# Performance work log

Hardware: AMD Instinct MI355X
Metric: run time of the kernel (lower is better)

The kernel has to match this reference:

```python
import jax, jax.numpy as jnp
from jax import lax
import numpy as np

EPS = 1e-5


def setup_inputs() -> dict:
    key = jax.random.key(0)
    ks = jax.random.split(key, 12)
    S, N, C, V = 512, 64, 512, 10
    sc = 1.0 / np.sqrt(C)
    inp = {
        "memory": jax.random.normal(ks[0], (S, N, C), jnp.float32),
        "W_act": jax.random.normal(ks[1], (C, 2), jnp.float32) * sc,
        "b_act": jnp.zeros((2,), jnp.float32),
        "W_ih": jax.random.normal(ks[2], (4 * C, C), jnp.float32) * sc,
        "W_hh": jax.random.normal(ks[3], (4 * C, C), jnp.float32) * sc,
        "b_ih": jnp.zeros((4 * C,), jnp.float32),
        "b_hh": jnp.zeros((4 * C,), jnp.float32),
        "ln_gamma": jnp.ones((C,), jnp.float32),
        "ln_beta": jnp.zeros((C,), jnp.float32),
        "W_dec": jax.random.normal(ks[4], (C, V), jnp.float32) * sc,
        "b_dec": jnp.zeros((V,), jnp.float32),
        "qsize": 256,
    }
    return inp


def reference(memory, W_act, b_act, W_ih, W_hh, b_ih, b_hh,
              ln_gamma, ln_beta, W_dec, b_dec, qsize):
    S, N, C = memory.shape
    # action probabilities (training path: plain softmax), [S, N, 2]
    actions = jax.nn.softmax(memory @ W_act + b_act, axis=-1)

    # posvec linear recurrence: p_{i+1} = p_i * a0_i + roll(p_i, 1) * a1_i
    p0 = jnp.zeros((qsize, N), memory.dtype).at[0].set(1.0)

    def pos_step(p, a):  # a: [N, 2]
        p_next = p * a[:, 0] + jnp.roll(p, 1, axis=0) * a[:, 1]
        return p_next, p  # emit posvec BEFORE update (used at step i)

    _, posvecs = lax.scan(pos_step, p0, actions)  # [S, qsize, N]

    # queue = sum_i outer(posvec_i, memory_i) * a1_i  -> [qsize, N, C]
    queue = jnp.einsum('sqn,snc,sn->qnc', posvecs, memory, actions[..., 1])

    # single-layer LSTM over the queue dimension (PyTorch gate order i,f,g,o)
    h0 = jnp.zeros((N, C), memory.dtype)

    def lstm_step(carry, x):  # x: [N, C]
        h, c = carry
        gates = x @ W_ih.T + h @ W_hh.T + b_ih + b_hh  # [N, 4C]
        i, f, g, o = jnp.split(gates, 4, axis=-1)
        c = jax.nn.sigmoid(f) * c + jax.nn.sigmoid(i) * jnp.tanh(g)
        h = jax.nn.sigmoid(o) * jnp.tanh(c)
        return (h, c), h

    _, hs = lax.scan(lstm_step, (h0, h0), queue)  # [qsize, N, C]

    # dropout is identity in eval / reference mode
    mu = jnp.mean(hs, axis=-1, keepdims=True)
    var = jnp.mean(jnp.square(hs - mu), axis=-1, keepdims=True)
    normed = (hs - mu) * lax.rsqrt(var + EPS) * ln_gamma + ln_beta

    return normed @ W_dec + b_dec  # [qsize, N, V]
```

## Files before the change

### kernel.cpp

```cpp
#include <hip/hip_runtime.h>
#include <hip/hip_bf16.h>

typedef __bf16 bf16;
typedef __bf16 bf16x8 __attribute__((ext_vector_type(8)));
typedef float f32x4 __attribute__((ext_vector_type(4)));
typedef float f32x16 __attribute__((ext_vector_type(16)));

#define S_ 512
#define N_ 64
#define C_ 512
#define V_ 10
#define Q_ 256

#define OFF_A0   ((size_t)0)
#define OFF_A1   (OFF_A0 + (size_t)S_ * N_ * 4)
#define OFF_PW   (OFF_A1 + (size_t)S_ * N_ * 4)
#define OFF_QU   (OFF_PW + (size_t)N_ * Q_ * S_ * 2)
#define OFF_H    (OFF_QU + (size_t)Q_ * N_ * C_ * 2)
#define OFF_HS   (OFF_H + (size_t)2 * N_ * C_ * 2)
#define OFF_BAR  (OFF_HS + (size_t)Q_ * N_ * C_ * 2)

__device__ __forceinline__ float sigf(float x) { return 1.f / (1.f + __expf(-x)); }
__device__ __forceinline__ float tanhf_(float x) { return 1.f - 2.f / (__expf(2.f * x) + 1.f); }

__global__ __launch_bounds__(256) void k_actions(const float* __restrict__ mem,
    const float* __restrict__ Wact, const float* __restrict__ bact,
    float* __restrict__ A0, float* __restrict__ A1) {
  const int wid = threadIdx.x >> 6, lane = threadIdx.x & 63;
  const int row = blockIdx.x * 4 + wid;
  const int s = row >> 6, n = row & 63;
  const float* mrow = mem + (size_t)row * C_ + lane * 8;
  const float* wrow = Wact + (size_t)lane * 16;
  float4 m0 = *(const float4*)(mrow);
  float4 m1 = *(const float4*)(mrow + 4);
  float d0 = 0.f, d1 = 0.f;
  float mv[8] = {m0.x, m0.y, m0.z, m0.w, m1.x, m1.y, m1.z, m1.w};
#pragma unroll
  for (int j = 0; j < 8; ++j) {
    d0 += mv[j] * wrow[j * 2 + 0];
    d1 += mv[j] * wrow[j * 2 + 1];
  }
#pragma unroll
  for (int m = 32; m >= 1; m >>= 1) {
    d0 += __shfl_xor(d0, m);
    d1 += __shfl_xor(d1, m);
  }
  if (lane == 0) {
    float l0 = d0 + bact[0], l1 = d1 + bact[1];
    float mx = fmaxf(l0, l1);
    float e0 = __expf(l0 - mx), e1 = __expf(l1 - mx);
    float inv = 1.f / (e0 + e1);
    A0[(size_t)n * S_ + s] = e0 * inv;
    A1[(size_t)n * S_ + s] = e1 * inv;
  }
}

__global__ __launch_bounds__(256) void k_posvec(const float* __restrict__ A0,
    const float* __restrict__ A1, bf16* __restrict__ Pw) {
  __shared__ float a0s[S_], a1s[S_];
  __shared__ float pbuf[2][Q_];
  const int n = blockIdx.x, t = threadIdx.x;
  a0s[t] = A0[(size_t)n * S_ + t];
  a0s[t + 256] = A0[(size_t)n * S_ + t + 256];
  a1s[t] = A1[(size_t)n * S_ + t];
  a1s[t + 256] = A1[(size_t)n * S_ + t + 256];
  float p = (t == 0) ? 1.f : 0.f;
  __syncthreads();
  for (int s8 = 0; s8 < S_; s8 += 8) {
    float emit[8];
#pragma unroll
    for (int jj = 0; jj < 8; ++jj) {
      const int s = s8 + jj;
      pbuf[jj & 1][t] = p;
      __syncthreads();
      float pm1 = pbuf[jj & 1][(t + Q_ - 1) & (Q_ - 1)];
      float a0 = a0s[s], a1 = a1s[s];
      emit[jj] = p * a1;
      p = fmaf(pm1, a1, p * a0);
    }
    bf16x8 v;
#pragma unroll
    for (int jj = 0; jj < 8; ++jj) v[jj] = (bf16)emit[jj];
    *(bf16x8*)(Pw + ((size_t)n * Q_ + t) * S_ + s8) = v;
  }
}

__global__ __launch_bounds__(256) void k_queue(const bf16* __restrict__ Pw,
    const float* __restrict__ mem, bf16* __restrict__ qout) {
  __shared__ bf16 bt[64 * 32];
  const int bid = blockIdx.x;
  const int n = bid >> 5, qt = (bid >> 3) & 3, ct = bid & 7;
  const int q0 = qt * 64, c0 = ct * 64;
  const int t = threadIdx.x, wid = t >> 6, lane = t & 63;
  const int lrow = lane & 15, lkb = lane >> 4;
  f32x4 acc[4] = {};
  const bf16* arow = Pw + ((size_t)n * Q_ + q0 + wid * 16 + lrow) * S_ + lkb * 8;
  const int sl = t >> 3, cb = (t & 7) * 8;
  const float* msrc = mem + ((size_t)sl * N_ + n) * C_ + c0 + cb;
  for (int kb = 0; kb < 16; ++kb) {
    float4 f0 = *(const float4*)(msrc + (size_t)kb * 32 * N_ * C_);
    float4 f1 = *(const float4*)(msrc + (size_t)kb * 32 * N_ * C_ + 4);
    __syncthreads();
    float fv[8] = {f0.x, f0.y, f0.z, f0.w, f1.x, f1.y, f1.z, f1.w};
#pragma unroll
    for (int jw = 0; jw < 8; ++jw) {
      const int row = cb + jw;
      bt[row * 32 + ((((sl >> 3) ^ (row & 3)) << 3) | (sl & 7))] = (bf16)fv[jw];
    }
    __syncthreads();
    bf16x8 a = *(const bf16x8*)(arow + kb * 32);
#pragma unroll
    for (int cs = 0; cs < 4; ++cs) {
      const int row = cs * 16 + lrow;
      bf16x8 b = *(const bf16x8*)(&bt[row * 32 + ((lkb ^ (row & 3)) << 3)]);
      acc[cs] = __builtin_amdgcn_mfma_f32_16x16x32_bf16(a, b, acc[cs], 0, 0, 0);
    }
  }
#pragma unroll
  for (int cs = 0; cs < 4; ++cs) {
#pragma unroll
    for (int r = 0; r < 4; ++r) {
      const int q = q0 + wid * 16 + (lane >> 4) * 4 + r;
      const int c = c0 + cs * 16 + lrow;
      qout[((size_t)q * N_ + n) * C_ + c] = (bf16)acc[cs][r];
    }
  }
}

__global__ __launch_bounds__(256, 1) void k_lstm(
    const bf16* __restrict__ queue, const float* __restrict__ Wih,
    const float* __restrict__ Whh, const float* __restrict__ bih,
    const float* __restrict__ bhh, bf16* __restrict__ H,
    bf16* __restrict__ hs, int* __restrict__ ctrl) {
  const int bid = blockIdx.x, t = threadIdx.x;

  if (bid >= 64) {
    float x0 = 1.f + t, x1 = 2.f + t, x2 = 3.f + t, x3 = 4.f + t;
    for (int outer = 0; outer < 10000; ++outer) {
      int d;
      asm volatile("global_load_dword %0, %1, off sc0 sc1" : "=v"(d) : "v"(ctrl));
#pragma unroll
      for (int i = 0; i < 500; ++i) {
        x0 = fmaf(x0, 0.9999999f, 1e-7f);
        x1 = fmaf(x1, 0.9999998f, 2e-7f);
        x2 = fmaf(x2, 1.0000001f, 3e-7f);
        x3 = fmaf(x3, 1.0000002f, 4e-7f);
      }
      asm volatile("s_waitcnt vmcnt(0)" ::: "memory");
      if (d) break;
    }
    asm volatile("" :: "v"(x0), "v"(x1), "v"(x2), "v"(x3));
    return;
  }

  __shared__ float gx[2][2][32][33];
  __shared__ float gh[2][32][33];
  __shared__ float bias[32];
  __shared__ int ldsCnt[Q_];
  __shared__ int ldsCnt0;
  int* flags = ctrl + 64;
  const int w = bid;
  const int wid = t >> 6, lane = t & 63;
  const int mat = wid >> 1;
  const int blk = wid & 1;

  const int col = lane & 31;
  const int kg = (lane >> 5) * 8;
  const int wr = (col & 3) * 512 + w * 8 + (col >> 2);
  const float* Wsrc = (mat ? Whh : Wih) + (size_t)wr * C_ + kg;
  bf16x8 bw[32];
#pragma unroll
  for (int kb = 0; kb < 32; ++kb) {
    float4 wa = *(const float4*)(Wsrc + kb * 16);
    float4 wb = *(const float4*)(Wsrc + kb * 16 + 4);
    bf16x8 v;
    v[0] = (bf16)wa.x; v[1] = (bf16)wa.y; v[2] = (bf16)wa.z; v[3] = (bf16)wa.w;
    v[4] = (bf16)wb.x; v[5] = (bf16)wb.y; v[6] = (bf16)wb.z; v[7] = (bf16)wb.w;
    bw[kb] = v;
  }
  if (t < 32) {
    const int rr = (t & 3) * 512 + w * 8 + (t >> 2);
    bias[t] = bih[rr] + bhh[rr];
  }
  ldsCnt[t] = 0;
  if (t == 0) ldsCnt0 = 0;
  __syncthreads();

  const int en = t >> 2, ep = t & 3;
  {
    unsigned* Hp = (unsigned*)H + ((size_t)0 * N_ + en) * (C_ / 2) + w * 4 + ep;
    unsigned z = 0;
    asm volatile("global_store_dword %0, %1, off sc0 sc1" :: "v"(Hp), "v"(z) : "memory");
    asm volatile("s_waitcnt vmcnt(0)" ::: "memory");
    if (lane == 0) {
      if (atomicAdd(&ldsCnt0, 1) == 3) {
        int one = 1;
        int* fp = flags + w;
        asm volatile("global_store_dword %0, %1, off sc0 sc1" :: "v"(fp), "v"(one) : "memory");
      }
    }
  }

  float cs0 = 0.f, cs1 = 0.f;
  const int eb = en >> 5, er = en & 31, j0 = ep * 8;

  bf16x8 xf[32];
  if (mat == 0) {
    const bf16* xb = queue + ((size_t)0 * N_ + blk * 32 + (lane & 31)) * C_ + kg;
#pragma unroll
    for (int kb = 0; kb < 32; ++kb) xf[kb] = *(const bf16x8*)(xb + kb * 16);
    {
      f32x16 acc[4] = {};
#pragma unroll
      for (int kb = 0; kb < 32; ++kb)
        acc[kb & 3] = __builtin_amdgcn_mfma_f32_32x32x16_bf16(xf[kb], bw[kb], acc[kb & 3], 0, 0, 0);
      f32x16 asum = (acc[0] + acc[1]) + (acc[2] + acc[3]);
#pragma unroll
      for (int rg = 0; rg < 16; ++rg) {
        const int rl = (rg & 3) + 8 * (rg >> 2) + 4 * (lane >> 5);
        gx[0][blk][rl][col] = asum[rg];
      }
    }
    const bf16* xb1 = queue + ((size_t)1 * N_ + blk * 32 + (lane & 31)) * C_ + kg;
#pragma unroll
    for (int kb = 0; kb < 32; ++kb) xf[kb] = *(const bf16x8*)(xb1 + kb * 16);
  }

  for (int step = 0; step < Q_; ++step) {
    const int p = step & 1;
    const int cur = p, nxt = p ^ 1;
    if (mat == 1) {
      {
        int v;
        int* fa = flags + lane;
        do {
          asm volatile("global_load_dword %0, %1, off sc0 sc1" : "=v"(v) : "v"(fa));
          asm volatile("s_waitcnt vmcnt(0)" ::: "memory");
        } while (!__all(v >= step + 1));
      }
      __builtin_amdgcn_sched_barrier(0);
      const bf16* hb = H + ((size_t)cur * N_ + blk * 32 + (lane & 31)) * C_ + kg;
      bf16x8 hf[32];
#pragma unroll
      for (int kb = 0; kb < 32; ++kb)
        asm volatile("global_load_dwordx4 %0, %1, off offset:%2 sc0 sc1"
                     : "=v"(hf[kb]) : "v"(hb), "i"(kb * 32));
      f32x16 acc[4] = {};
      asm volatile("s_waitcnt vmcnt(24)" ::: "memory");
      __builtin_amdgcn_sched_barrier(0);
#pragma unroll
      for (int kb = 0; kb < 8; ++kb)
        acc[kb & 3] = __builtin_amdgcn_mfma_f32_32x32x16_bf16(hf[kb], bw[kb], acc[kb & 3], 0, 0, 0);
      asm volatile("s_waitcnt vmcnt(16)" ::: "memory");
      __builtin_amdgcn_sched_barrier(0);
#pragma unroll
      for (int kb = 8; kb < 16; ++kb)
        acc[kb & 3] = __builtin_amdgcn_mfma_f32_32x32x16_bf16(hf[kb], bw[kb], acc[kb & 3], 0, 0, 0);
      asm volatile("s_waitcnt vmcnt(8)" ::: "memory");
      __builtin_amdgcn_sched_barrier(0);
#pragma unroll
      for (int kb = 16; kb < 24; ++kb)
        acc[kb & 3] = __builtin_amdgcn_mfma_f32_32x32x16_bf16(hf[kb], bw[kb], acc[kb & 3], 0, 0, 0);
      asm volatile("s_waitcnt vmcnt(0)" ::: "memory");
      __builtin_amdgcn_sched_barrier(0);
#pragma unroll
      for (int kb = 24; kb < 32; ++kb)
        acc[kb & 3] = __builtin_amdgcn_mfma_f32_32x32x16_bf16(hf[kb], bw[kb], acc[kb & 3], 0, 0, 0);
      f32x16 asum = (acc[0] + acc[1]) + (acc[2] + acc[3]);
#pragma unroll
      for (int rg = 0; rg < 16; ++rg) {
        const int rl = (rg & 3) + 8 * (rg >> 2) + 4 * (lane >> 5);
        gh[blk][rl][col] = asum[rg];
      }
    } else if (step + 1 < Q_) {
      f32x16 acc[4] = {};
#pragma unroll
      for (int kb = 0; kb < 32; ++kb)
        acc[kb & 3] = __builtin_amdgcn_mfma_f32_32x32x16_bf16(xf[kb], bw[kb], acc[kb & 3], 0, 0, 0);
      f32x16 asum = (acc[0] + acc[1]) + (acc[2] + acc[3]);
#pragma unroll
      for (int rg = 0; rg < 16; ++rg) {
        const int rl = (rg & 3) + 8 * (rg >> 2) + 4 * (lane >> 5);
        gx[p ^ 1][blk][rl][col] = asum[rg];
      }
    }
    __syncthreads();

    {
      float g0 = gx[p][eb][er][j0 + 0] + gh[eb][er][j0 + 0] + bias[j0 + 0];
      float g1 = gx[p][eb][er][j0 + 1] + gh[eb][er][j0 + 1] + bias[j0 + 1];
      float g2 = gx[p][eb][er][j0 + 2] + gh[eb][er][j0 + 2] + bias[j0 + 2];
      float g3 = gx[p][eb][er][j0 + 3] + gh[eb][er][j0 + 3] + bias[j0 + 3];
      cs0 = sigf(g1) * cs0 + sigf(g0) * tanhf_(g2);
      float h0v = sigf(g3) * tanhf_(cs0);
      float g4 = gx[p][eb][er][j0 + 4] + gh[eb][er][j0 + 4] + bias[j0 + 4];
      float g5 = gx[p][eb][er][j0 + 5] + gh[eb][er][j0 + 5] + bias[j0 + 5];
      float g6 = gx[p][eb][er][j0 + 6] + gh[eb][er][j0 + 6] + bias[j0 + 6];
      float g7 = gx[p][eb][er][j0 + 7] + gh[eb][er][j0 + 7] + bias[j0 + 7];
      cs1 = sigf(g5) * cs1 + sigf(g4) * tanhf_(g6);
      float h1v = sigf(g7) * tanhf_(cs1);
      unsigned lo = __builtin_bit_cast(unsigned short, (bf16)h0v);
      unsigned hi = __builtin_bit_cast(unsigned short, (bf16)h1v);
      unsigned hp = (hi << 16) | lo;
      unsigned* Hp = (unsigned*)H + ((size_t)nxt * N_ + en) * (C_ / 2) + w * 4 + ep;
      asm volatile("global_store_dword %0, %1, off sc0 sc1" :: "v"(Hp), "v"(hp) : "memory");
      *((unsigned*)hs + ((size_t)step * N_ + en) * (C_ / 2) + w * 4 + ep) = hp;
    }
    asm volatile("s_waitcnt vmcnt(1)" ::: "memory");
    if (step + 1 < Q_) {
      if (lane == 0) {
        if (atomicAdd(&ldsCnt[step], 1) == 3) {
          int fv = step + 2;
          int* fp = flags + w;
          asm volatile("global_store_dword %0, %1, off sc0 sc1" :: "v"(fp), "v"(fv) : "memory");
        }
      }
      if (mat == 0 && step + 2 < Q_) {
        const bf16* xb = queue + ((size_t)(step + 2) * N_ + blk * 32 + (lane & 31)) * C_ + kg;
#pragma unroll
        for (int kb = 0; kb < 32; ++kb) xf[kb] = *(const bf16x8*)(xb + kb * 16);
      }
    }
    __syncthreads();
  }

  if (t == 0 && bid == 0) {
    int one = 1;
    asm volatile("global_store_dword %0, %1, off sc0 sc1" :: "v"(ctrl), "v"(one) : "memory");
  }
}

__global__ __launch_bounds__(256) void k_lndec(const bf16* __restrict__ hs,
    const float* __restrict__ gamma, const float* __restrict__ beta,
    const float* __restrict__ Wdec, const float* __restrict__ bdec,
    float* __restrict__ out) {
  const int wid = threadIdx.x >> 6, lane = threadIdx.x & 63;
  const int row = blockIdx.x * 4 + wid;
  const bf16* hrow = hs + (size_t)row * C_ + lane * 8;
  bf16x8 hv = *(const bf16x8*)hrow;
  float h[8];
  float sm = 0.f, sq = 0.f;
#pragma unroll
  for (int j = 0; j < 8; ++j) {
    h[j] = (float)hv[j];
    sm += h[j];
    sq += h[j] * h[j];
  }
#pragma unroll
  for (int m = 32; m >= 1; m >>= 1) {
    sm += __shfl_xor(sm, m);
    sq += __shfl_xor(sq, m);
  }
  const float mu = sm * (1.f / C_);
  const float var = sq * (1.f / C_) - mu * mu;
  const float rs = 1.f / sqrtf(var + 1e-5f);
  float o[V_] = {};
#pragma unroll
  for (int j = 0; j < 8; ++j) {
    const int cj = lane * 8 + j;
    const float nv = (h[j] - mu) * rs * gamma[cj] + beta[cj];
    const float* wr = Wdec + (size_t)cj * V_;
#pragma unroll
    for (int v = 0; v < V_; ++v) o[v] += nv * wr[v];
  }
#pragma unroll
  for (int v = 0; v < V_; ++v) {
#pragma unroll
    for (int m = 32; m >= 1; m >>= 1) o[v] += __shfl_xor(o[v], m);
  }
  if (lane == 0) {
#pragma unroll
    for (int v = 0; v < V_; ++v) out[(size_t)row * V_ + v] = o[v] + bdec[v];
  }
}

extern "C" void kernel_launch(void* const* d_in, const int* in_sizes, int n_in,
                              void* d_out, int out_size, void* d_ws, size_t ws_size,
                              hipStream_t stream) {
  (void)in_sizes; (void)n_in; (void)out_size; (void)ws_size;
  const float* mem  = (const float*)d_in[0];
  const float* Wact = (const float*)d_in[1];
  const float* bact = (const float*)d_in[2];
  const float* Wih  = (const float*)d_in[3];
  const float* Whh  = (const float*)d_in[4];
  const float* bih  = (const float*)d_in[5];
  const float* bhh  = (const float*)d_in[6];
  const float* gam  = (const float*)d_in[7];
  const float* bet  = (const float*)d_in[8];
  const float* Wdec = (const float*)d_in[9];
  const float* bdec = (const float*)d_in[10];
  float* out = (float*)d_out;

  char* ws = (char*)d_ws;
  float* A0 = (float*)(ws + OFF_A0);
  float* A1 = (float*)(ws + OFF_A1);
  bf16* Pw  = (bf16*)(ws + OFF_PW);
  bf16* qu  = (bf16*)(ws + OFF_QU);
  bf16* H   = (bf16*)(ws + OFF_H);
  bf16* hs  = (bf16*)(ws + OFF_HS);
  int* ctrl = (int*)(ws + OFF_BAR);

  hipMemsetAsync(ctrl, 0, 4096, stream);
  k_actions<<<(S_ * N_) / 4, 256, 0, stream>>>(mem, Wact, bact, A0, A1);
  k_posvec<<<N_, 256, 0, stream>>>(A0, A1, Pw);
  k_queue<<<N_ * 32, 256, 0, stream>>>(Pw, mem, qu);
  k_lstm<<<256, 256, 0, stream>>>(qu, Wih, Whh, bih, bhh, H, hs, ctrl);
  k_lndec<<<(Q_ * N_) / 4, 256, 0, stream>>>(hs, gam, bet, Wdec, bdec, out);
}
```

Baseline: 1.675 ms.

## Replace LSTM step flags with step-tagged hidden-state words and chunked validation

The hidden state is now stored as 32-bit words, each carrying a bf16 value in the low half and the step number in the high half. Consumer warps load it in double-buffered chunks and re-issue a chunk until every tag matches, instead of waiting on a per-step flag and then fetching the data. This removes one global round trip per recurrence step; the remaining per-block progress counter is only a coarse hint, and its spin loop is now bounded. The 192 busy-spinning filler blocks are removed and the grid shrinks to 64 blocks, which may change clock behaviour. The trade-off is doubled hidden-state traffic and fewer MFMA accumulator chains.

```diff
diff --git a/kernel.cpp b/kernel.cpp
--- a/kernel.cpp
+++ b/kernel.cpp
@@ -16,9 +16,9 @@
 #define OFF_A1   (OFF_A0 + (size_t)S_ * N_ * 4)
 #define OFF_PW   (OFF_A1 + (size_t)S_ * N_ * 4)
 #define OFF_QU   (OFF_PW + (size_t)N_ * Q_ * S_ * 2)
-#define OFF_H    (OFF_QU + (size_t)Q_ * N_ * C_ * 2)
-#define OFF_HS   (OFF_H + (size_t)2 * N_ * C_ * 2)
-#define OFF_BAR  (OFF_HS + (size_t)Q_ * N_ * C_ * 2)
+#define OFF_HP   (OFF_QU + (size_t)Q_ * N_ * C_ * 2)
+#define OFF_HS   (OFF_HP + (size_t)2 * N_ * C_ * 4)
+#define OFF_CTRL (OFF_HS + (size_t)Q_ * N_ * C_ * 2)
 
 __device__ __forceinline__ float sigf(float x) { return 1.f / (1.f + __expf(-x)); }
 __device__ __forceinline__ float tanhf_(float x) { return 1.f - 2.f / (__expf(2.f * x) + 1.f); }
@@ -127,39 +127,68 @@
   }
 }
 
+
+#define ISSUE_CHUNK(BUF, C8)                                                    \
+  {                                                                             \
+    _Pragma("unroll") for (int i_ = 0; i_ < 8; ++i_)                            \
+        asm volatile("global_load_dwordx4 %0, %1, off offset:%2 sc0 sc1"        \
+                     : "=v"(BUF[i_])                                            \
+                     : "v"(hb), "i"(((C8) * 4 + (i_ >> 1)) * 64 + (i_ & 1) * 16)); \
+  }
+
+#define CHECK_CHUNK(BUF, OKV)                                                   \
+  {                                                                             \
+    unsigned a_ = 0;                                                            \
+    _Pragma("unroll") for (int i_ = 0; i_ < 8; ++i_) {                          \
+      a_ |= (BUF[i_].x ^ want); a_ |= (BUF[i_].y ^ want);                       \
+      a_ |= (BUF[i_].z ^ want); a_ |= (BUF[i_].w ^ want);                       \
+    }                                                                           \
+    OKV = (a_ < 0x10000u);                                                      \
+  }
+
+#define CONSUME_CHUNK(BUF, C8)                                                  \
+  {                                                                             \
+    _Pragma("unroll") for (int k_ = 0; k_ < 4; ++k_) {                          \
+      union { unsigned u[4]; bf16x8 v; } cv_;                                   \
+      cv_.u[0] = (BUF[k_ * 2].y << 16) | (BUF[k_ * 2].x & 0xffffu);             \
+      cv_.u[1] = (BUF[k_ * 2].w << 16) | (BUF[k_ * 2].z & 0xffffu);             \
+      cv_.u[2] = (BUF[k_ * 2 + 1].y << 16) | (BUF[k_ * 2 + 1].x & 0xffffu);     \
+      cv_.u[3] = (BUF[k_ * 2 + 1].w << 16) | (BUF[k_ * 2 + 1].z & 0xffffu);     \
+      const int kb_ = (C8) * 4 + k_;                                            \
+      acc[kb_ & 1] = __builtin_amdgcn_mfma_f32_32x32x16_bf16(cv_.v, bw[kb_],    \
+                                                             acc[kb_ & 1], 0, 0, 0); \
+    }                                                                           \
+  }
+
+#define CHUNK_STEP(C8, X, Y)                                                    \
+  {                                                                             \
+    if ((C8) < 7) {                                                             \
+      ISSUE_CHUNK(Y, (C8) + 1);                                                 \
+      asm volatile("s_waitcnt vmcnt(8)" ::: "memory");                          \
+    } else {                                                                    \
+      asm volatile("s_waitcnt vmcnt(0)" ::: "memory");                          \
+    }                                                                           \
+    __builtin_amdgcn_sched_barrier(0);                                          \
+    int ok_;                                                                    \
+    CHECK_CHUNK(X, ok_);                                                        \
+    while (!__all(ok_)) {                                                       \
+      ISSUE_CHUNK(X, C8);                                                       \
+      asm volatile("s_waitcnt vmcnt(0)" ::: "memory");                          \
+      __builtin_amdgcn_sched_barrier(0);                                        \
+      CHECK_CHUNK(X, ok_);                                                      \
+    }                                                                           \
+    CONSUME_CHUNK(X, C8)                                                        \
+  }
+
 __global__ __launch_bounds__(256, 1) void k_lstm(
     const bf16* __restrict__ queue, const float* __restrict__ Wih,
     const float* __restrict__ Whh, const float* __restrict__ bih,
-    const float* __restrict__ bhh, bf16* __restrict__ H,
-    bf16* __restrict__ hs, int* __restrict__ ctrl) {
-  const int bid = blockIdx.x, t = threadIdx.x;
-
-  if (bid >= 64) {
-    float x0 = 1.f + t, x1 = 2.f + t, x2 = 3.f + t, x3 = 4.f + t;
-    for (int outer = 0; outer < 10000; ++outer) {
-      int d;
-      asm volatile("global_load_dword %0, %1, off sc0 sc1" : "=v"(d) : "v"(ctrl));
-#pragma unroll
-      for (int i = 0; i < 500; ++i) {
-        x0 = fmaf(x0, 0.9999999f, 1e-7f);
-        x1 = fmaf(x1, 0.9999998f, 2e-7f);
-        x2 = fmaf(x2, 1.0000001f, 3e-7f);
-        x3 = fmaf(x3, 1.0000002f, 4e-7f);
-      }
-      asm volatile("s_waitcnt vmcnt(0)" ::: "memory");
-      if (d) break;
-    }
-    asm volatile("" :: "v"(x0), "v"(x1), "v"(x2), "v"(x3));
-    return;
-  }
-
+    const float* __restrict__ bhh, unsigned* __restrict__ Hp,
+    bf16* __restrict__ hs, int* __restrict__ summ) {
   __shared__ float gx[2][2][32][33];
   __shared__ float gh[2][32][33];
   __shared__ float bias[32];
-  __shared__ int ldsCnt[Q_];
-  __shared__ int ldsCnt0;
-  int* flags = ctrl + 64;
-  const int w = bid;
+  const int w = blockIdx.x, t = threadIdx.x;
   const int wid = t >> 6, lane = t & 63;
   const int mat = wid >> 1;
   const int blk = wid & 1;
@@ -182,23 +211,16 @@
     const int rr = (t & 3) * 512 + w * 8 + (t >> 2);
     bias[t] = bih[rr] + bhh[rr];
   }
-  ldsCnt[t] = 0;
-  if (t == 0) ldsCnt0 = 0;
-  __syncthreads();
 
   const int en = t >> 2, ep = t & 3;
   {
-    unsigned* Hp = (unsigned*)H + ((size_t)0 * N_ + en) * (C_ / 2) + w * 4 + ep;
-    unsigned z = 0;
-    asm volatile("global_store_dword %0, %1, off sc0 sc1" :: "v"(Hp), "v"(z) : "memory");
+    uint2 z0; z0.x = 0u; z0.y = 0u;
+    uint2 z1; z1.x = 0xFFFF0000u; z1.y = 0xFFFF0000u;
+    unsigned* p0 = Hp + ((size_t)0 * N_ + en) * C_ + w * 8 + ep * 2;
+    unsigned* p1 = Hp + ((size_t)1 * N_ + en) * C_ + w * 8 + ep * 2;
+    asm volatile("global_store_dwordx2 %0, %1, off sc0 sc1" :: "v"(p0), "v"(z0) : "memory");
+    asm volatile("global_store_dwordx2 %0, %1, off sc0 sc1" :: "v"(p1), "v"(z1) : "memory");
     asm volatile("s_waitcnt vmcnt(0)" ::: "memory");
-    if (lane == 0) {
-      if (atomicAdd(&ldsCnt0, 1) == 3) {
-        int one = 1;
-        int* fp = flags + w;
-        asm volatile("global_store_dword %0, %1, off sc0 sc1" :: "v"(fp), "v"(one) : "memory");
-      }
-    }
   }
 
   float cs0 = 0.f, cs1 = 0.f;
@@ -210,11 +232,11 @@
 #pragma unroll
     for (int kb = 0; kb < 32; ++kb) xf[kb] = *(const bf16x8*)(xb + kb * 16);
     {
-      f32x16 acc[4] = {};
+      f32x16 acc[2] = {};
 #pragma unroll
       for (int kb = 0; kb < 32; ++kb)
-        acc[kb & 3] = __builtin_amdgcn_mfma_f32_32x32x16_bf16(xf[kb], bw[kb], acc[kb & 3], 0, 0, 0);
-      f32x16 asum = (acc[0] + acc[1]) + (acc[2] + acc[3]);
+        acc[kb & 1] = __builtin_amdgcn_mfma_f32_32x32x16_bf16(xf[kb], bw[kb], acc[kb & 1], 0, 0, 0);
+      f32x16 asum = acc[0] + acc[1];
 #pragma unroll
       for (int rg = 0; rg < 16; ++rg) {
         const int rl = (rg & 3) + 8 * (rg >> 2) + 4 * (lane >> 5);
@@ -231,53 +253,39 @@
     const int cur = p, nxt = p ^ 1;
     if (mat == 1) {
       {
-        int v;
-        int* fa = flags + lane;
+        int v, it = 0;
+        const int* fa = summ + lane;
         do {
           asm volatile("global_load_dword %0, %1, off sc0 sc1" : "=v"(v) : "v"(fa));
           asm volatile("s_waitcnt vmcnt(0)" ::: "memory");
-        } while (!__all(v >= step + 1));
+        } while (__any(v < step) && ++it < 16384);
       }
       __builtin_amdgcn_sched_barrier(0);
-      const bf16* hb = H + ((size_t)cur * N_ + blk * 32 + (lane & 31)) * C_ + kg;
-      bf16x8 hf[32];
-#pragma unroll
-      for (int kb = 0; kb < 32; ++kb)
-        asm volatile("global_load_dwordx4 %0, %1, off offset:%2 sc0 sc1"
-                     : "=v"(hf[kb]) : "v"(hb), "i"(kb * 32));
-      f32x16 acc[4] = {};
-      asm volatile("s_waitcnt vmcnt(24)" ::: "memory");
-      __builtin_amdgcn_sched_barrier(0);
-#pragma unroll
-      for (int kb = 0; kb < 8; ++kb)
-        acc[kb & 3] = __builtin_amdgcn_mfma_f32_32x32x16_bf16(hf[kb], bw[kb], acc[kb & 3], 0, 0, 0);
-      asm volatile("s_waitcnt vmcnt(16)" ::: "memory");
-      __builtin_amdgcn_sched_barrier(0);
-#pragma unroll
-      for (int kb = 8; kb < 16; ++kb)
-        acc[kb & 3] = __builtin_amdgcn_mfma_f32_32x32x16_bf16(hf[kb], bw[kb], acc[kb & 3], 0, 0, 0);
-      asm volatile("s_waitcnt vmcnt(8)" ::: "memory");
-      __builtin_amdgcn_sched_barrier(0);
-#pragma unroll
-      for (int kb = 16; kb < 24; ++kb)
-        acc[kb & 3] = __builtin_amdgcn_mfma_f32_32x32x16_bf16(hf[kb], bw[kb], acc[kb & 3], 0, 0, 0);
-      asm volatile("s_waitcnt vmcnt(0)" ::: "memory");
-      __builtin_amdgcn_sched_barrier(0);
-#pragma unroll
-      for (int kb = 24; kb < 32; ++kb)
-        acc[kb & 3] = __builtin_amdgcn_mfma_f32_32x32x16_bf16(hf[kb], bw[kb], acc[kb & 3], 0, 0, 0);
-      f32x16 asum = (acc[0] + acc[1]) + (acc[2] + acc[3]);
+      const unsigned want = (unsigned)step << 16;
+      unsigned* hb = Hp + ((size_t)cur * N_ + blk * 32 + (lane & 31)) * C_ + kg;
+      f32x16 acc[2] = {};
+      uint4 ba[8], bb[8];
+      ISSUE_CHUNK(ba, 0);
+      CHUNK_STEP(0, ba, bb);
+      CHUNK_STEP(1, bb, ba);
+      CHUNK_STEP(2, ba, bb);
+      CHUNK_STEP(3, bb, ba);
+      CHUNK_STEP(4, ba, bb);
+      CHUNK_STEP(5, bb, ba);
+      CHUNK_STEP(6, ba, bb);
+      CHUNK_STEP(7, bb, ba);
+      f32x16 asum = acc[0] + acc[1];
 #pragma unroll
       for (int rg = 0; rg < 16; ++rg) {
         const int rl = (rg & 3) + 8 * (rg >> 2) + 4 * (lane >> 5);
         gh[blk][rl][col] = asum[rg];
       }
     } else if (step + 1 < Q_) {
-      f32x16 acc[4] = {};
+      f32x16 acc[2] = {};
 #pragma unroll
       for (int kb = 0; kb < 32; ++kb)
-        acc[kb & 3] = __builtin_amdgcn_mfma_f32_32x32x16_bf16(xf[kb], bw[kb], acc[kb & 3], 0, 0, 0);
-      f32x16 asum = (acc[0] + acc[1]) + (acc[2] + acc[3]);
+        acc[kb & 1] = __builtin_amdgcn_mfma_f32_32x32x16_bf16(xf[kb], bw[kb], acc[kb & 1], 0, 0, 0);
+      f32x16 asum = acc[0] + acc[1];
 #pragma unroll
       for (int rg = 0; rg < 16; ++rg) {
         const int rl = (rg & 3) + 8 * (rg >> 2) + 4 * (lane >> 5);
@@ -299,34 +307,24 @@
       float g7 = gx[p][eb][er][j0 + 7] + gh[eb][er][j0 + 7] + bias[j0 + 7];
       cs1 = sigf(g5) * cs1 + sigf(g4) * tanhf_(g6);
       float h1v = sigf(g7) * tanhf_(cs1);
-      unsigned lo = __builtin_bit_cast(unsigned short, (bf16)h0v);
-      unsigned hi = __builtin_bit_cast(unsigned short, (bf16)h1v);
-      unsigned hp = (hi << 16) | lo;
-      unsigned* Hp = (unsigned*)H + ((size_t)nxt * N_ + en) * (C_ / 2) + w * 4 + ep;
-      asm volatile("global_store_dword %0, %1, off sc0 sc1" :: "v"(Hp), "v"(hp) : "memory");
-      *((unsigned*)hs + ((size_t)step * N_ + en) * (C_ / 2) + w * 4 + ep) = hp;
-    }
-    asm volatile("s_waitcnt vmcnt(1)" ::: "memory");
-    if (step + 1 < Q_) {
-      if (lane == 0) {
-        if (atomicAdd(&ldsCnt[step], 1) == 3) {
-          int fv = step + 2;
-          int* fp = flags + w;
-          asm volatile("global_store_dword %0, %1, off sc0 sc1" :: "v"(fp), "v"(fv) : "memory");
-        }
-      }
-      if (mat == 0 && step + 2 < Q_) {
-        const bf16* xb = queue + ((size_t)(step + 2) * N_ + blk * 32 + (lane & 31)) * C_ + kg;
-#pragma unroll
-        for (int kb = 0; kb < 32; ++kb) xf[kb] = *(const bf16x8*)(xb + kb * 16);
-      }
+      unsigned lo = (unsigned)__builtin_bit_cast(unsigned short, (bf16)h0v);
+      unsigned hi = (unsigned)__builtin_bit_cast(unsigned short, (bf16)h1v);
+      const unsigned tagv = (unsigned)(step + 1) << 16;
+      uint2 pr; pr.x = tagv | lo; pr.y = tagv | hi;
+      unsigned* Hq = Hp + ((size_t)nxt * N_ + en) * C_ + w * 8 + ep * 2;
+      asm volatile("global_store_dwordx2 %0, %1, off sc0 sc1" :: "v"(Hq), "v"(pr) : "memory");
+      *((unsigned*)hs + ((size_t)step * N_ + en) * (C_ / 2) + w * 4 + ep) = (hi << 16) | lo;
+    }
+    if (mat == 0 && step + 2 < Q_) {
+      const bf16* xb = queue + ((size_t)(step + 2) * N_ + blk * 32 + (lane & 31)) * C_ + kg;
+#pragma unroll
+      for (int kb = 0; kb < 32; ++kb) xf[kb] = *(const bf16x8*)(xb + kb * 16);
     }
     __syncthreads();
-  }
-
-  if (t == 0 && bid == 0) {
-    int one = 1;
-    asm volatile("global_store_dword %0, %1, off sc0 sc1" :: "v"(ctrl), "v"(one) : "memory");
+    if (t == 0 && step + 1 < Q_) {
+      int sv = step + 1; int* sp = summ + w;
+      asm volatile("global_store_dword %0, %1, off sc0 sc1" :: "v"(sp), "v"(sv) : "memory");
+    }
   }
 }
 
@@ -392,18 +390,18 @@
   float* out = (float*)d_out;
 
   char* ws = (char*)d_ws;
-  float* A0 = (float*)(ws + OFF_A0);
-  float* A1 = (float*)(ws + OFF_A1);
-  bf16* Pw  = (bf16*)(ws + OFF_PW);
-  bf16* qu  = (bf16*)(ws + OFF_QU);
-  bf16* H   = (bf16*)(ws + OFF_H);
-  bf16* hs  = (bf16*)(ws + OFF_HS);
-  int* ctrl = (int*)(ws + OFF_BAR);
+  float* A0    = (float*)(ws + OFF_A0);
+  float* A1    = (float*)(ws + OFF_A1);
+  bf16* Pw     = (bf16*)(ws + OFF_PW);
+  bf16* qu     = (bf16*)(ws + OFF_QU);
+  unsigned* Hp = (unsigned*)(ws + OFF_HP);
+  bf16* hs     = (bf16*)(ws + OFF_HS);
+  int* ctrl    = (int*)(ws + OFF_CTRL);
 
   hipMemsetAsync(ctrl, 0, 4096, stream);
   k_actions<<<(S_ * N_) / 4, 256, 0, stream>>>(mem, Wact, bact, A0, A1);
   k_posvec<<<N_, 256, 0, stream>>>(A0, A1, Pw);
   k_queue<<<N_ * 32, 256, 0, stream>>>(Pw, mem, qu);
-  k_lstm<<<256, 256, 0, stream>>>(qu, Wih, Whh, bih, bhh, H, hs, ctrl);
+  k_lstm<<<64, 256, 0, stream>>>(qu, Wih, Whh, bih, bhh, Hp, hs, ctrl);
   k_lndec<<<(Q_ * N_) / 4, 256, 0, stream>>>(hs, gam, bet, Wdec, bdec, out);
 }
```

Result: slower. 2.470 ms (+47.4%).

## Drop spinner blocks and use single-waiter flag sync with scattered history buffer

Applied to the files above, without the earlier changes.

Removes the 192 dummy spinning blocks that kept clocks up and launches only the 64 working blocks. The h exchange moves from a 2-slot ping-pong buffer to a per-step history buffer scattered with a stride-97 permutation. Synchronisation changes so that one wave polls the flags with s_sleep and a block barrier releases the rest. The h loads become plain chunked loads instead of asm-pipelined waits. The intent is to cut power and memory contention from the spinners and to simplify the handshake, at the risk of lower clocks and added barrier latency on the critical serial path.

```diff
diff --git a/kernel.cpp b/kernel.cpp
--- a/kernel.cpp
+++ b/kernel.cpp
@@ -16,9 +16,9 @@
 #define OFF_A1   (OFF_A0 + (size_t)S_ * N_ * 4)
 #define OFF_PW   (OFF_A1 + (size_t)S_ * N_ * 4)
 #define OFF_QU   (OFF_PW + (size_t)N_ * Q_ * S_ * 2)
-#define OFF_H    (OFF_QU + (size_t)Q_ * N_ * C_ * 2)
-#define OFF_HS   (OFF_H + (size_t)2 * N_ * C_ * 2)
-#define OFF_BAR  (OFF_HS + (size_t)Q_ * N_ * C_ * 2)
+#define OFF_HSEQ (OFF_QU + (size_t)Q_ * N_ * C_ * 2)
+#define OFF_HS   (OFF_HSEQ + (size_t)Q_ * N_ * C_ * 2)
+#define OFF_CTRL (OFF_HS + (size_t)Q_ * N_ * C_ * 2)
 
 __device__ __forceinline__ float sigf(float x) { return 1.f / (1.f + __expf(-x)); }
 __device__ __forceinline__ float tanhf_(float x) { return 1.f - 2.f / (__expf(2.f * x) + 1.f); }
@@ -130,36 +130,14 @@
 __global__ __launch_bounds__(256, 1) void k_lstm(
     const bf16* __restrict__ queue, const float* __restrict__ Wih,
     const float* __restrict__ Whh, const float* __restrict__ bih,
-    const float* __restrict__ bhh, bf16* __restrict__ H,
+    const float* __restrict__ bhh, bf16* __restrict__ Hseq,
     bf16* __restrict__ hs, int* __restrict__ ctrl) {
-  const int bid = blockIdx.x, t = threadIdx.x;
-
-  if (bid >= 64) {
-    float x0 = 1.f + t, x1 = 2.f + t, x2 = 3.f + t, x3 = 4.f + t;
-    for (int outer = 0; outer < 10000; ++outer) {
-      int d;
-      asm volatile("global_load_dword %0, %1, off sc0 sc1" : "=v"(d) : "v"(ctrl));
-#pragma unroll
-      for (int i = 0; i < 500; ++i) {
-        x0 = fmaf(x0, 0.9999999f, 1e-7f);
-        x1 = fmaf(x1, 0.9999998f, 2e-7f);
-        x2 = fmaf(x2, 1.0000001f, 3e-7f);
-        x3 = fmaf(x3, 1.0000002f, 4e-7f);
-      }
-      asm volatile("s_waitcnt vmcnt(0)" ::: "memory");
-      if (d) break;
-    }
-    asm volatile("" :: "v"(x0), "v"(x1), "v"(x2), "v"(x3));
-    return;
-  }
-
   __shared__ float gx[2][2][32][33];
   __shared__ float gh[2][32][33];
   __shared__ float bias[32];
   __shared__ int ldsCnt[Q_];
-  __shared__ int ldsCnt0;
   int* flags = ctrl + 64;
-  const int w = bid;
+  const int w = blockIdx.x, t = threadIdx.x;
   const int wid = t >> 6, lane = t & 63;
   const int mat = wid >> 1;
   const int blk = wid & 1;
@@ -183,25 +161,10 @@
     bias[t] = bih[rr] + bhh[rr];
   }
   ldsCnt[t] = 0;
-  if (t == 0) ldsCnt0 = 0;
   __syncthreads();
 
+  float cs0 = 0.f, cs1 = 0.f;
   const int en = t >> 2, ep = t & 3;
-  {
-    unsigned* Hp = (unsigned*)H + ((size_t)0 * N_ + en) * (C_ / 2) + w * 4 + ep;
-    unsigned z = 0;
-    asm volatile("global_store_dword %0, %1, off sc0 sc1" :: "v"(Hp), "v"(z) : "memory");
-    asm volatile("s_waitcnt vmcnt(0)" ::: "memory");
-    if (lane == 0) {
-      if (atomicAdd(&ldsCnt0, 1) == 3) {
-        int one = 1;
-        int* fp = flags + w;
-        asm volatile("global_store_dword %0, %1, off sc0 sc1" :: "v"(fp), "v"(one) : "memory");
-      }
-    }
-  }
-
-  float cs0 = 0.f, cs1 = 0.f;
   const int eb = en >> 5, er = en & 31, j0 = ep * 8;
 
   bf16x8 xf[32];
@@ -228,44 +191,35 @@
 
   for (int step = 0; step < Q_; ++step) {
     const int p = step & 1;
-    const int cur = p, nxt = p ^ 1;
+    if (wid == 2 && step > 0) {
+      int v;
+      int* fa = flags + lane;
+      while (true) {
+        asm volatile("global_load_dword %0, %1, off sc0 sc1" : "=v"(v) : "v"(fa));
+        asm volatile("s_waitcnt vmcnt(0)" ::: "memory");
+        if (__all(v >= step)) break;
+        __builtin_amdgcn_s_sleep(1);
+      }
+    }
+    __syncthreads();
+
     if (mat == 1) {
-      {
-        int v;
-        int* fa = flags + lane;
-        do {
-          asm volatile("global_load_dword %0, %1, off sc0 sc1" : "=v"(v) : "v"(fa));
-          asm volatile("s_waitcnt vmcnt(0)" ::: "memory");
-        } while (!__all(v >= step + 1));
-      }
-      __builtin_amdgcn_sched_barrier(0);
-      const bf16* hb = H + ((size_t)cur * N_ + blk * 32 + (lane & 31)) * C_ + kg;
-      bf16x8 hf[32];
-#pragma unroll
-      for (int kb = 0; kb < 32; ++kb)
-        asm volatile("global_load_dwordx4 %0, %1, off offset:%2 sc0 sc1"
-                     : "=v"(hf[kb]) : "v"(hb), "i"(kb * 32));
       f32x16 acc[4] = {};
-      asm volatile("s_waitcnt vmcnt(24)" ::: "memory");
-      __builtin_amdgcn_sched_barrier(0);
-#pragma unroll
-      for (int kb = 0; kb < 8; ++kb)
-        acc[kb & 3] = __builtin_amdgcn_mfma_f32_32x32x16_bf16(hf[kb], bw[kb], acc[kb & 3], 0, 0, 0);
-      asm volatile("s_waitcnt vmcnt(16)" ::: "memory");
-      __builtin_amdgcn_sched_barrier(0);
-#pragma unroll
-      for (int kb = 8; kb < 16; ++kb)
-        acc[kb & 3] = __builtin_amdgcn_mfma_f32_32x32x16_bf16(hf[kb], bw[kb], acc[kb & 3], 0, 0, 0);
-      asm volatile("s_waitcnt vmcnt(8)" ::: "memory");
-      __builtin_amdgcn_sched_barrier(0);
-#pragma unroll
-      for (int kb = 16; kb < 24; ++kb)
-        acc[kb & 3] = __builtin_amdgcn_mfma_f32_32x32x16_bf16(hf[kb], bw[kb], acc[kb & 3], 0, 0, 0);
-      asm volatile("s_waitcnt vmcnt(0)" ::: "memory");
-      __builtin_amdgcn_sched_barrier(0);
-#pragma unroll
-      for (int kb = 24; kb < 32; ++kb)
-        acc[kb & 3] = __builtin_amdgcn_mfma_f32_32x32x16_bf16(hf[kb], bw[kb], acc[kb & 3], 0, 0, 0);
+      if (step > 0) {
+        const int sp = ((step - 1) * 97) & 255;
+        const bf16* hrow = Hseq + ((size_t)sp * N_ + blk * 32 + (lane & 31)) * C_ + kg;
+#pragma unroll
+        for (int c8 = 0; c8 < 4; ++c8) {
+          bf16x8 hf[8];
+#pragma unroll
+          for (int kk = 0; kk < 8; ++kk) hf[kk] = *(const bf16x8*)(hrow + (c8 * 8 + kk) * 16);
+#pragma unroll
+          for (int kk = 0; kk < 8; ++kk) {
+            const int kb = c8 * 8 + kk;
+            acc[kb & 3] = __builtin_amdgcn_mfma_f32_32x32x16_bf16(hf[kk], bw[kb], acc[kb & 3], 0, 0, 0);
+          }
+        }
+      }
       f32x16 asum = (acc[0] + acc[1]) + (acc[2] + acc[3]);
 #pragma unroll
       for (int rg = 0; rg < 16; ++rg) {
@@ -299,18 +253,19 @@
       float g7 = gx[p][eb][er][j0 + 7] + gh[eb][er][j0 + 7] + bias[j0 + 7];
       cs1 = sigf(g5) * cs1 + sigf(g4) * tanhf_(g6);
       float h1v = sigf(g7) * tanhf_(cs1);
-      unsigned lo = __builtin_bit_cast(unsigned short, (bf16)h0v);
-      unsigned hi = __builtin_bit_cast(unsigned short, (bf16)h1v);
+      unsigned lo = (unsigned)__builtin_bit_cast(unsigned short, (bf16)h0v);
+      unsigned hi = (unsigned)__builtin_bit_cast(unsigned short, (bf16)h1v);
       unsigned hp = (hi << 16) | lo;
-      unsigned* Hp = (unsigned*)H + ((size_t)nxt * N_ + en) * (C_ / 2) + w * 4 + ep;
-      asm volatile("global_store_dword %0, %1, off sc0 sc1" :: "v"(Hp), "v"(hp) : "memory");
+      const int spw = (step * 97) & 255;
+      unsigned* Hq = (unsigned*)Hseq + ((size_t)spw * N_ + en) * (C_ / 2) + w * 4 + ep;
+      asm volatile("global_store_dword %0, %1, off sc0 sc1" :: "v"(Hq), "v"(hp) : "memory");
       *((unsigned*)hs + ((size_t)step * N_ + en) * (C_ / 2) + w * 4 + ep) = hp;
     }
-    asm volatile("s_waitcnt vmcnt(1)" ::: "memory");
+    asm volatile("s_waitcnt vmcnt(0)" ::: "memory");
     if (step + 1 < Q_) {
       if (lane == 0) {
         if (atomicAdd(&ldsCnt[step], 1) == 3) {
-          int fv = step + 2;
+          int fv = step + 1;
           int* fp = flags + w;
           asm volatile("global_store_dword %0, %1, off sc0 sc1" :: "v"(fp), "v"(fv) : "memory");
         }
@@ -322,11 +277,6 @@
       }
     }
     __syncthreads();
-  }
-
-  if (t == 0 && bid == 0) {
-    int one = 1;
-    asm volatile("global_store_dword %0, %1, off sc0 sc1" :: "v"(ctrl), "v"(one) : "memory");
   }
 }
 
@@ -392,18 +342,18 @@
   float* out = (float*)d_out;
 
   char* ws = (char*)d_ws;
-  float* A0 = (float*)(ws + OFF_A0);
-  float* A1 = (float*)(ws + OFF_A1);
-  bf16* Pw  = (bf16*)(ws + OFF_PW);
-  bf16* qu  = (bf16*)(ws + OFF_QU);
-  bf16* H   = (bf16*)(ws + OFF_H);
-  bf16* hs  = (bf16*)(ws + OFF_HS);
-  int* ctrl = (int*)(ws + OFF_BAR);
+  float* A0  = (float*)(ws + OFF_A0);
+  float* A1  = (float*)(ws + OFF_A1);
+  bf16* Pw   = (bf16*)(ws + OFF_PW);
+  bf16* qu   = (bf16*)(ws + OFF_QU);
+  bf16* Hsq  = (bf16*)(ws + OFF_HSEQ);
+  bf16* hs   = (bf16*)(ws + OFF_HS);
+  int* ctrl  = (int*)(ws + OFF_CTRL);
 
   hipMemsetAsync(ctrl, 0, 4096, stream);
   k_actions<<<(S_ * N_) / 4, 256, 0, stream>>>(mem, Wact, bact, A0, A1);
   k_posvec<<<N_, 256, 0, stream>>>(A0, A1, Pw);
   k_queue<<<N_ * 32, 256, 0, stream>>>(Pw, mem, qu);
-  k_lstm<<<256, 256, 0, stream>>>(qu, Wih, Whh, bih, bhh, H, hs, ctrl);
+  k_lstm<<<64, 256, 0, stream>>>(qu, Wih, Whh, bih, bhh, Hsq, hs, ctrl);
   k_lndec<<<(Q_ * N_) / 4, 256, 0, stream>>>(hs, gam, bet, Wdec, bdec, out);
 }
```

New measurement: 2.194 ms. 31.0% more time.
